# Kernel optimization log

Hardware: AMD Instinct MI355X
Metric: run time of the kernel (lower is better)

## Reference

```python
import jax, jax.numpy as jnp
import numpy as np

N, E, B, D, R, L = 60000, 600000, 512, 128, 30, 3
CUT_LOW, CUT_HIGH = 0.0, 10.0
N_ATOM_TYPES = 100


def _sp(x, beta, threshold):
    # torch.nn.Softplus(beta, threshold): x if beta*x > threshold else log1p(exp(beta*x))/beta
    bx = beta * x
    return jnp.where(bx > threshold, x, jnp.log1p(jnp.exp(jnp.minimum(bx, threshold))) / beta)


def setup_inputs() -> dict:
    key = jax.random.key(0)
    ks = jax.random.split(key, 16)

    def lin(k, fi, fo):
        k1, k2 = jax.random.split(k)
        W = jax.random.normal(k1, (fi, fo), jnp.float32) * (fi ** -0.5)
        b = jax.random.normal(k2, (fo,), jnp.float32) * 0.01
        return W, b

    def lin_stack(k, fi, fo, n):
        Ws, bs = zip(*[lin(kk, fi, fo) for kk in jax.random.split(k, n)])
        return jnp.stack(Ws), jnp.stack(bs)

    inp = {}
    inp['atom_type'] = jax.random.randint(ks[0], (N,), 0, N_ATOM_TYPES)
    inp['src'] = jax.random.randint(ks[1], (E,), 0, N)
    inp['dst'] = jax.random.randint(ks[2], (E,), 0, N)
    inp['graph_ids'] = jnp.sort(jax.random.randint(ks[3], (N,), 0, B))
    inp['dist'] = jax.random.uniform(ks[4], (E,), jnp.float32) * CUT_HIGH
    inp['node_emb'] = jax.random.normal(ks[5], (N_ATOM_TYPES, D), jnp.float32) * 0.1
    inp['W_n1'], inp['b_n1'] = lin_stack(ks[6], D, D, L)
    inp['W_c1'], inp['b_c1'] = lin_stack(ks[7], R, D, L)
    inp['W_c2'], inp['b_c2'] = lin_stack(ks[8], D, D, L)
    inp['W_c3'], inp['b_c3'] = lin_stack(ks[9], D, D, L)
    inp['W_n2'], inp['b_n2'] = lin_stack(ks[10], D, D, L)
    inp['W_n3'], inp['b_n3'] = lin_stack(ks[11], D, D, L)
    inp['W_r1'], inp['b_r1'] = lin(ks[12], D * (L + 1), 64)
    inp['W_r2'], inp['b_r2'] = lin(ks[13], 64, 1)
    return inp


def reference(atom_type, src, dst, graph_ids, dist, node_emb,
              W_n1, b_n1, W_c1, b_c1, W_c2, b_c2, W_c3, b_c3,
              W_n2, b_n2, W_n3, b_n3, W_r1, b_r1, W_r2, b_r2):
    # RBF expansion of edge distances: exp(-(d - mu_k)^2 / gap)  -> [E, R]
    centers = jnp.linspace(CUT_LOW, CUT_HIGH, R).astype(dist.dtype)
    gap = centers[1] - centers[0]
    rbf = jnp.exp(-((dist[:, None] - centers) ** 2) / gap)

    h = node_emb[atom_type]  # node embedding lookup [N, D]
    hs = [h]
    for i in range(L):  # MultiLevelInteraction layers (fixed small count)
        h_new = hs[-1] @ W_n1[i] + b_n1[i]                       # node_layer1 [N, D]
        # VEConv edge MLP on rbf (linear1 -> softplus(0.5,14) -> linear2 -> linear3)
        e = _sp(rbf @ W_c1[i] + b_c1[i], 0.5, 14.0) @ W_c2[i] + b_c2[i]
        e = e @ W_c3[i] + b_c3[i]                                 # [E, D]
        # sum_e(h_new[src]*e) + sum_e(e) fused into one scatter-sum over dst
        msg = (h_new[src] + 1.0) * e                              # [E, D]
        node = jax.ops.segment_sum(msg, dst, num_segments=N)      # [N, D]
        new_node = _sp(node @ W_n2[i] + b_n2[i], 0.5, 14.0) @ W_n3[i] + b_n3[i]
        hs.append(hs[-1] + new_node)                              # residual h_i
    hcat = jnp.concatenate(hs, axis=1)                            # [N, D*(L+1)]
    out = _sp(hcat @ W_r1 + b_r1, 1.0, 20.0) @ W_r2 + b_r2        # [N, 1]
    # dgl.sum_nodes per molecule, then flatten -> [B]
    return jax.ops.segment_sum(out[:, 0], graph_ids, num_segments=B)
```

## Files before the change

kernel.cpp:

```cpp
#include <hip/hip_runtime.h>
#include <math.h>

#define N_NODES 60000
#define N_EDGES 600000
#define B_GRAPHS 512
#define DIM 128
#define RBF_R 30
#define NLAYERS 3
#define NBINS 4096
#define CHUNK 512
#define NCHUNK ((N_NODES + CHUNK - 1) / CHUNK)

typedef __attribute__((ext_vector_type(8))) short bf16x8;
typedef __attribute__((ext_vector_type(4))) float f32x4;

__device__ __forceinline__ float sp05(float x) {
    float bx = 0.5f * x;
    return bx > 14.0f ? x : 2.0f * log1pf(expf(bx));
}
__device__ __forceinline__ float sp1(float x) {
    return x > 20.0f ? x : log1pf(expf(x));
}
__device__ __forceinline__ unsigned short f2bf(float f) {
    unsigned int u = __float_as_uint(f);
    unsigned int r = u + 0x7FFFu + ((u >> 16) & 1u);
    return (unsigned short)(r >> 16);
}
__device__ __forceinline__ float bf2f(unsigned short s) {
    return __uint_as_float(((unsigned int)s) << 16);
}


__global__ void k_convW(const float* __restrict__ Wn1, const float* __restrict__ Wn2,
                        const float* __restrict__ Wn3, unsigned short* __restrict__ WtF) {
    int i = blockIdx.x * 256 + threadIdx.x;
    int mat = i >> 14, r = i & 16383;
    int frag = r >> 9, within = r & 511;
    int ks = frag >> 3, ntile = frag & 7;
    int lane = within >> 3, j = within & 7;
    int q = lane >> 4, l16 = lane & 15;
    int n = ntile * 16 + l16;
    int k = ks * 32 + q * 8 + j;
    const float* src = (mat < 3) ? (Wn1 + (size_t)mat * 16384)
                     : (mat < 6) ? (Wn2 + (size_t)(mat - 3) * 16384)
                                 : (Wn3 + (size_t)(mat - 6) * 16384);
    WtF[i] = f2bf(src[k * 128 + n]);
}

__global__ void k_convR(const float* __restrict__ Wr1, unsigned short* __restrict__ Wr1tF) {
    int i = blockIdx.x * 256 + threadIdx.x;
    int frag = i >> 9, within = i & 511;
    int lvl = frag >> 4, ks = (frag >> 2) & 3, ntile = frag & 3;
    int lane = within >> 3, j = within & 7;
    int q = lane >> 4, l16 = lane & 15;
    int n = ntile * 16 + l16;
    int k = lvl * 128 + ks * 32 + q * 8 + j;
    Wr1tF[i] = f2bf(Wr1[k * 64 + n]);
}

__global__ void k_embed(const int* __restrict__ atom_type,
                        const float* __restrict__ node_emb,
                        float* __restrict__ h0, unsigned short* __restrict__ hb0) {
    int i = blockIdx.x * blockDim.x + threadIdx.x;
    if (i >= N_NODES * DIM) return;
    int n = i >> 7, d = i & 127;
    float v = node_emb[atom_type[n] * DIM + d];
    h0[i] = v;
    hb0[i] = f2bf(v);
}


__global__ void k_hist(const int* __restrict__ dst, int* __restrict__ counts) {
    int e = blockIdx.x * blockDim.x + threadIdx.x;
    if (e >= N_EDGES) return;
    atomicAdd(&counts[dst[e]], 1);
}

__global__ void k_bsum(const int* __restrict__ counts, int* __restrict__ bsums) {
    __shared__ int red[256];
    int c = blockIdx.x, tid = threadIdx.x;
    int base = c * CHUNK;
    int v = 0;
    for (int i = tid; i < CHUNK; i += 256)
        if (base + i < N_NODES) v += counts[base + i];
    red[tid] = v;
    __syncthreads();
    for (int s = 128; s > 0; s >>= 1) {
        if (tid < s) red[tid] += red[tid + s];
        __syncthreads();
    }
    if (tid == 0) bsums[c] = red[0];
}

__global__ void k_scan_b(int* __restrict__ bsums) {
    __shared__ int sb[NCHUNK];
    int tid = threadIdx.x;
    if (tid < NCHUNK) sb[tid] = bsums[tid];
    __syncthreads();
    if (tid == 0) {
        int run = 0;
        for (int i = 0; i < NCHUNK; ++i) { int v = sb[i]; sb[i] = run; run += v; }
    }
    __syncthreads();
    if (tid < NCHUNK) bsums[tid] = sb[tid];
}

__global__ void k_scan_final(const int* __restrict__ counts, const int* __restrict__ bsums,
                             int* __restrict__ offsets) {
    __shared__ int sc[CHUNK];
    int c = blockIdx.x, tid = threadIdx.x;
    int base = c * CHUNK;
    for (int i = tid; i < CHUNK; i += 256)
        sc[i] = (base + i < N_NODES) ? counts[base + i] : 0;
    __syncthreads();
    if (tid == 0) {
        int run = bsums[c];
        for (int i = 0; i < CHUNK; ++i) { int v = sc[i]; sc[i] = run; run += v; }
    }
    __syncthreads();
    for (int i = tid; i < CHUNK; i += 256)
        if (base + i < N_NODES) offsets[base + i] = sc[i];
    if (c == 0 && tid == 0) offsets[N_NODES] = N_EDGES;
}

__global__ void k_fill(const int* __restrict__ src, const int* __restrict__ dst,
                       const float* __restrict__ dist,
                       const int* __restrict__ offsets, int* __restrict__ cnt2,
                       int* __restrict__ srcp, int* __restrict__ binp,
                       float* __restrict__ wp) {
    int e = blockIdx.x * blockDim.x + threadIdx.x;
    if (e >= N_EDGES) return;
    int d = dst[e];
    int pos = offsets[d] + atomicAdd(&cnt2[d], 1);
    srcp[pos] = src[e];
    float x = dist[e];
    float p = x * ((float)NBINS / 10.0f);
    int bin = (int)p;
    if (bin > NBINS - 1) bin = NBINS - 1;
    binp[pos] = bin;
    wp[pos] = p - (float)bin;
}


__global__ void k_table(const float* __restrict__ Wc1, const float* __restrict__ bc1,
                        const float* __restrict__ Wc2, const float* __restrict__ bc2,
                        const float* __restrict__ Wc3, const float* __restrict__ bc3,
                        unsigned short* __restrict__ tableb) {
    __shared__ float t[DIM];
    __shared__ float u[DIM];
    int b = blockIdx.x;
    int d = threadIdx.x;
    float dist = (float)b * (10.0f / (float)NBINS);
    const float gap = 10.0f / 29.0f;
    float acc = bc1[d];
#pragma unroll
    for (int k = 0; k < RBF_R; ++k) {
        float c = (float)k * (10.0f / 29.0f);
        float df = dist - c;
        acc += expf(-df * df / gap) * Wc1[k * DIM + d];
    }
    t[d] = sp05(acc);
    __syncthreads();
    acc = bc2[d];
#pragma unroll 8
    for (int k = 0; k < DIM; ++k) acc += t[k] * Wc2[k * DIM + d];
    u[d] = acc;
    __syncthreads();
    acc = bc3[d];
#pragma unroll 8
    for (int k = 0; k < DIM; ++k) acc += u[k] * Wc3[k * DIM + d];
    tableb[b * DIM + d] = f2bf(acc);
}

__global__ __launch_bounds__(256) void k_gemm_g(const unsigned short* __restrict__ Ab,
                                                const unsigned short* __restrict__ WtF,
                                                const float* __restrict__ bias,
                                                unsigned short* __restrict__ Cb) {
    int tid = threadIdx.x;
    int wave = tid >> 6, lane = tid & 63;
    int q = lane >> 4, l16 = lane & 15;
    int mhalf = wave & 1, nhalf = wave >> 1;
    int rb = blockIdx.x * 64 + mhalf * 32;
    int c0 = nhalf * 64;
    bf16x8 bfrag[4][4];
#pragma unroll
    for (int ks = 0; ks < 4; ++ks)
#pragma unroll
        for (int nt = 0; nt < 4; ++nt)
            bfrag[ks][nt] = *(const bf16x8*)&WtF[(size_t)(ks * 8 + nhalf * 4 + nt) * 512 + lane * 8];
    f32x4 acc[2][4] = {};
#pragma unroll
    for (int ks = 0; ks < 4; ++ks)
#pragma unroll
        for (int mt = 0; mt < 2; ++mt) {
            int m = rb + mt * 16 + l16;
            if (m > N_NODES - 1) m = N_NODES - 1;
            bf16x8 a = *(const bf16x8*)&Ab[(size_t)m * 128 + ks * 32 + q * 8];
#pragma unroll
            for (int nt = 0; nt < 4; ++nt)
                acc[mt][nt] = __builtin_amdgcn_mfma_f32_16x16x32_bf16(a, bfrag[ks][nt], acc[mt][nt], 0, 0, 0);
        }
#pragma unroll
    for (int mt = 0; mt < 2; ++mt)
#pragma unroll
        for (int nt = 0; nt < 4; ++nt) {
            int col = c0 + nt * 16 + l16;
            float b = bias[col] + 1.0f;
#pragma unroll
            for (int r = 0; r < 4; ++r) {
                int row = rb + mt * 16 + q * 4 + r;
                if (row < N_NODES) Cb[(size_t)row * 128 + col] = f2bf(acc[mt][nt][r] + b);
            }
        }
}

__global__ void k_gather(const int* __restrict__ offsets,
                         const int* __restrict__ srcp, const int* __restrict__ binp,
                         const float* __restrict__ wp,
                         const unsigned short* __restrict__ tableb,
                         const unsigned short* __restrict__ gb,
                         unsigned short* __restrict__ nodeb) {
    __shared__ int s_s[128];
    __shared__ int s_bin[128];
    __shared__ float s_w[128];
    int n = blockIdx.x;
    int d = threadIdx.x;
    int beg = offsets[n], end = offsets[n + 1];
    float acc = 0.0f;
    for (int base = beg; base < end; base += 128) {
        int cnt = min(128, end - base);
        if (d < cnt) {
            s_s[d] = srcp[base + d];
            s_bin[d] = binp[base + d];
            s_w[d] = wp[base + d];
        }
        __syncthreads();
        for (int j = 0; j < cnt; ++j) {
            int s = s_s[j];
            int bin = s_bin[j];
            float w = s_w[j];
            float a = bf2f(tableb[(size_t)bin * DIM + d]);
            float b = bf2f(tableb[(size_t)(bin + 1) * DIM + d]);
            float gv = bf2f(gb[(size_t)s * DIM + d]);
            acc += gv * (a + w * (b - a));
        }
        __syncthreads();
    }
    nodeb[(size_t)n * DIM + d] = f2bf(acc);
}

__global__ __launch_bounds__(256) void k_node_update(
    const unsigned short* __restrict__ nodeb,
    const unsigned short* __restrict__ W2tF, const float* __restrict__ b2,
    const unsigned short* __restrict__ W3tF, const float* __restrict__ b3,
    const float* __restrict__ h_in, float* __restrict__ h_out,
    unsigned short* __restrict__ hb_out) {
    __shared__ unsigned short ts[64][136];
    int tid = threadIdx.x;
    int wave = tid >> 6, lane = tid & 63;
    int q = lane >> 4, l16 = lane & 15;
    int mhalf = wave & 1, nhalf = wave >> 1;
    int rb = blockIdx.x * 64 + mhalf * 32;
    int c0 = nhalf * 64;

    bf16x8 bfrag[4][4];
#pragma unroll
    for (int ks = 0; ks < 4; ++ks)
#pragma unroll
        for (int nt = 0; nt < 4; ++nt)
            bfrag[ks][nt] = *(const bf16x8*)&W2tF[(size_t)(ks * 8 + nhalf * 4 + nt) * 512 + lane * 8];
    f32x4 acc[2][4] = {};
#pragma unroll
    for (int ks = 0; ks < 4; ++ks)
#pragma unroll
        for (int mt = 0; mt < 2; ++mt) {
            int m = rb + mt * 16 + l16;
            if (m > N_NODES - 1) m = N_NODES - 1;
            bf16x8 a = *(const bf16x8*)&nodeb[(size_t)m * 128 + ks * 32 + q * 8];
#pragma unroll
            for (int nt = 0; nt < 4; ++nt)
                acc[mt][nt] = __builtin_amdgcn_mfma_f32_16x16x32_bf16(a, bfrag[ks][nt], acc[mt][nt], 0, 0, 0);
        }
#pragma unroll
    for (int mt = 0; mt < 2; ++mt)
#pragma unroll
        for (int nt = 0; nt < 4; ++nt) {
            int col = c0 + nt * 16 + l16;
            float b = b2[col];
#pragma unroll
            for (int r = 0; r < 4; ++r) {
                int lrow = mhalf * 32 + mt * 16 + q * 4 + r;
                ts[lrow][col] = f2bf(sp05(acc[mt][nt][r] + b));
            }
        }
    __syncthreads();
#pragma unroll
    for (int ks = 0; ks < 4; ++ks)
#pragma unroll
        for (int nt = 0; nt < 4; ++nt)
            bfrag[ks][nt] = *(const bf16x8*)&W3tF[(size_t)(ks * 8 + nhalf * 4 + nt) * 512 + lane * 8];
#pragma unroll
    for (int mt = 0; mt < 2; ++mt)
#pragma unroll
        for (int nt = 0; nt < 4; ++nt) acc[mt][nt] = (f32x4){0.f, 0.f, 0.f, 0.f};
#pragma unroll
    for (int ks = 0; ks < 4; ++ks)
#pragma unroll
        for (int mt = 0; mt < 2; ++mt) {
            int lrow = mhalf * 32 + mt * 16 + l16;
            bf16x8 a = *(const bf16x8*)&ts[lrow][ks * 32 + q * 8];
#pragma unroll
            for (int nt = 0; nt < 4; ++nt)
                acc[mt][nt] = __builtin_amdgcn_mfma_f32_16x16x32_bf16(a, bfrag[ks][nt], acc[mt][nt], 0, 0, 0);
        }
#pragma unroll
    for (int mt = 0; mt < 2; ++mt)
#pragma unroll
        for (int nt = 0; nt < 4; ++nt) {
            int col = c0 + nt * 16 + l16;
            float b = b3[col];
#pragma unroll
            for (int r = 0; r < 4; ++r) {
                int row = rb + mt * 16 + q * 4 + r;
                if (row < N_NODES) {
                    size_t idx = (size_t)row * 128 + col;
                    float v = h_in[idx] + acc[mt][nt][r] + b;
                    h_out[idx] = v;
                    hb_out[idx] = f2bf(v);
                }
            }
        }
}

__global__ __launch_bounds__(256) void k_readout(
    const unsigned short* __restrict__ hb0, const unsigned short* __restrict__ hb1,
    const unsigned short* __restrict__ hb2, const unsigned short* __restrict__ hb3,
    const unsigned short* __restrict__ Wr1tF, const float* __restrict__ br1,
    const float* __restrict__ Wr2, const float* __restrict__ br2,
    const int* __restrict__ graph_ids, float* __restrict__ out) {
    int tid = threadIdx.x;
    int wave = tid >> 6, lane = tid & 63;
    int q = lane >> 4, l16 = lane & 15;
    int rb0 = blockIdx.x * 128 + wave * 16;
    const unsigned short* hbs[4] = {hb0, hb1, hb2, hb3};
    f32x4 acc[2][4] = {};
    for (int lvl = 0; lvl < 4; ++lvl) {
        bf16x8 bfrag[4][4];
#pragma unroll
        for (int ks = 0; ks < 4; ++ks)
#pragma unroll
            for (int nt = 0; nt < 4; ++nt)
                bfrag[ks][nt] = *(const bf16x8*)&Wr1tF[(size_t)((lvl * 4 + ks) * 4 + nt) * 512 + lane * 8];
        const unsigned short* Ab = hbs[lvl];
#pragma unroll
        for (int ks = 0; ks < 4; ++ks)
#pragma unroll
            for (int mt = 0; mt < 2; ++mt) {
                int m = rb0 + mt * 64 + l16;
                if (m > N_NODES - 1) m = N_NODES - 1;
                bf16x8 a = *(const bf16x8*)&Ab[(size_t)m * 128 + ks * 32 + q * 8];
#pragma unroll
                for (int nt = 0; nt < 4; ++nt)
                    acc[mt][nt] = __builtin_amdgcn_mfma_f32_16x16x32_bf16(a, bfrag[ks][nt], acc[mt][nt], 0, 0, 0);
            }
    }
    float brr = br2[0];
#pragma unroll
    for (int mt = 0; mt < 2; ++mt) {
        float partial[4] = {0.f, 0.f, 0.f, 0.f};
#pragma unroll
        for (int nt = 0; nt < 4; ++nt) {
            int col = nt * 16 + l16;
            float b = br1[col];
            float w = Wr2[col];
#pragma unroll
            for (int r = 0; r < 4; ++r) partial[r] += sp1(acc[mt][nt][r] + b) * w;
        }
#pragma unroll
        for (int r = 0; r < 4; ++r) {
            float v = partial[r];
            v += __shfl_xor(v, 1); v += __shfl_xor(v, 2);
            v += __shfl_xor(v, 4); v += __shfl_xor(v, 8);
            if (l16 == 0) {
                int row = rb0 + mt * 64 + q * 4 + r;
                if (row < N_NODES) atomicAdd(&out[graph_ids[row]], v + brr);
            }
        }
    }
}

extern "C" void kernel_launch(void* const* d_in, const int* in_sizes, int n_in,
                              void* d_out, int out_size, void* d_ws, size_t ws_size,
                              hipStream_t stream) {
    const int* atom_type   = (const int*)d_in[0];
    const int* src         = (const int*)d_in[1];
    const int* dst         = (const int*)d_in[2];
    const int* graph_ids   = (const int*)d_in[3];
    const float* dist      = (const float*)d_in[4];
    const float* node_emb  = (const float*)d_in[5];
    const float* W_n1 = (const float*)d_in[6];  const float* b_n1 = (const float*)d_in[7];
    const float* W_c1 = (const float*)d_in[8];  const float* b_c1 = (const float*)d_in[9];
    const float* W_c2 = (const float*)d_in[10]; const float* b_c2 = (const float*)d_in[11];
    const float* W_c3 = (const float*)d_in[12]; const float* b_c3 = (const float*)d_in[13];
    const float* W_n2 = (const float*)d_in[14]; const float* b_n2 = (const float*)d_in[15];
    const float* W_n3 = (const float*)d_in[16]; const float* b_n3 = (const float*)d_in[17];
    const float* W_r1 = (const float*)d_in[18]; const float* b_r1 = (const float*)d_in[19];
    const float* W_r2 = (const float*)d_in[20]; const float* b_r2 = (const float*)d_in[21];
    float* out = (float*)d_out;

    size_t ND = (size_t)N_NODES * DIM;
    float* h_even = (float*)d_ws;
    float* h_odd  = h_even + ND;
    float* wp     = h_odd + ND;
    int* offsets  = (int*)(wp + N_EDGES);
    int* srcp     = offsets + 60008;
    int* binp     = srcp + N_EDGES;
    int* counts   = binp + N_EDGES;
    int* cnt2     = counts + N_NODES;
    int* bsums    = cnt2 + N_NODES;
    unsigned short* hb0    = (unsigned short*)(bsums + 128);
    unsigned short* hb1    = hb0 + ND;
    unsigned short* hb2    = hb1 + ND;
    unsigned short* hb3    = hb2 + ND;
    unsigned short* gb     = hb3 + ND;
    unsigned short* nodeb  = gb + ND;
    unsigned short* tableb = nodeb + ND;
    unsigned short* WtF    = tableb + (size_t)(NBINS + 1) * DIM;
    unsigned short* Wr1tF  = WtF + 9 * 16384;

    unsigned short* hbp[4] = {hb0, hb1, hb2, hb3};
    float* hcur = h_even;
    float* hnext = h_odd;

    hipMemsetAsync(out, 0, B_GRAPHS * sizeof(float), stream);
    hipMemsetAsync(counts, 0, (2 * N_NODES + 128) * sizeof(int), stream);

    k_convW<<<(9 * 16384) / 256, 256, 0, stream>>>(W_n1, W_n2, W_n3, WtF);
    k_convR<<<32768 / 256, 256, 0, stream>>>(W_r1, Wr1tF);
    k_embed<<<(N_NODES * DIM) / 256, 256, 0, stream>>>(atom_type, node_emb, h_even, hb0);

    k_hist<<<(N_EDGES + 255) / 256, 256, 0, stream>>>(dst, counts);
    k_bsum<<<NCHUNK, 256, 0, stream>>>(counts, bsums);
    k_scan_b<<<1, 128, 0, stream>>>(bsums);
    k_scan_final<<<NCHUNK, 256, 0, stream>>>(counts, bsums, offsets);
    k_fill<<<(N_EDGES + 255) / 256, 256, 0, stream>>>(src, dst, dist, offsets, cnt2,
                                                      srcp, binp, wp);

    int gblocks = (N_NODES + 63) / 64;
    int rblocks = (N_NODES + 127) / 128;
    for (int i = 0; i < NLAYERS; ++i) {
        k_table<<<NBINS + 1, DIM, 0, stream>>>(
            W_c1 + (size_t)i * RBF_R * DIM, b_c1 + (size_t)i * DIM,
            W_c2 + (size_t)i * DIM * DIM,  b_c2 + (size_t)i * DIM,
            W_c3 + (size_t)i * DIM * DIM,  b_c3 + (size_t)i * DIM, tableb);
        k_gemm_g<<<gblocks, 256, 0, stream>>>(
            hbp[i], WtF + (size_t)i * 16384, b_n1 + (size_t)i * DIM, gb);
        k_gather<<<N_NODES, 128, 0, stream>>>(offsets, srcp, binp, wp, tableb, gb, nodeb);
        k_node_update<<<gblocks, 256, 0, stream>>>(
            nodeb, WtF + (size_t)(3 + i) * 16384, b_n2 + (size_t)i * DIM,
            WtF + (size_t)(6 + i) * 16384, b_n3 + (size_t)i * DIM,
            hcur, hnext, hbp[i + 1]);
        float* tmp = hcur; hcur = hnext; hnext = tmp;
    }
    k_readout<<<rblocks, 256, 0, stream>>>(
        hb0, hb1, hb2, hb3, Wr1tF, b_r1, W_r2, b_r2, graph_ids, out);
}
```

Baseline: 658.1 us.

## Shrink RBF table, pack interpolation pairs, wave-per-node gather, smaller readout tiles

Cuts the precomputed edge-filter table from 4096 to 1024 bins, which shrinks the per-layer table MLP work and keeps the table cache-resident. A new pack kernel stores each bin as a bf16 base value plus a bf16 delta to the next bin, so interpolation needs one 32-bit load. The gather kernel now assigns one wavefront per destination node, with each lane handling two features via 32-bit loads. It is unrolled two edges at a time and no longer uses shared memory or block barriers. Readout blocks now cover 64 rows instead of 128, giving more blocks; the coarser table and bf16 delta lower accuracy.

```diff
diff --git a/kernel.cpp b/kernel.cpp
--- a/kernel.cpp
+++ b/kernel.cpp
@@ -7,7 +7,7 @@
 #define DIM 128
 #define RBF_R 30
 #define NLAYERS 3
-#define NBINS 4096
+#define NBINS 1024
 #define CHUNK 512
 #define NCHUNK ((N_NODES + CHUNK - 1) / CHUNK)
 
@@ -26,8 +26,8 @@
     unsigned int r = u + 0x7FFFu + ((u >> 16) & 1u);
     return (unsigned short)(r >> 16);
 }
-__device__ __forceinline__ float bf2f(unsigned short s) {
-    return __uint_as_float(((unsigned int)s) << 16);
+__device__ __forceinline__ float bf2f(unsigned int s) {
+    return __uint_as_float(s << 16);
 }
 
 
@@ -172,6 +172,14 @@
     tableb[b * DIM + d] = f2bf(acc);
 }
 
+__global__ void k_pack(const unsigned short* __restrict__ tableb,
+                       unsigned int* __restrict__ packed) {
+    int i = blockIdx.x * 256 + threadIdx.x;
+    float a = bf2f(tableb[i]);
+    float b = bf2f(tableb[i + DIM]);
+    packed[i] = (unsigned int)f2bf(a) | ((unsigned int)f2bf(b - a) << 16);
+}
+
 __global__ __launch_bounds__(256) void k_gemm_g(const unsigned short* __restrict__ Ab,
                                                 const unsigned short* __restrict__ WtF,
                                                 const float* __restrict__ bias,
@@ -214,39 +222,41 @@
         }
 }
 
-__global__ void k_gather(const int* __restrict__ offsets,
-                         const int* __restrict__ srcp, const int* __restrict__ binp,
-                         const float* __restrict__ wp,
-                         const unsigned short* __restrict__ tableb,
-                         const unsigned short* __restrict__ gb,
-                         unsigned short* __restrict__ nodeb) {
-    __shared__ int s_s[128];
-    __shared__ int s_bin[128];
-    __shared__ float s_w[128];
-    int n = blockIdx.x;
-    int d = threadIdx.x;
+__global__ __launch_bounds__(256) void k_gather(
+    const int* __restrict__ offsets, const int* __restrict__ srcp,
+    const int* __restrict__ binp, const float* __restrict__ wp,
+    const unsigned int* __restrict__ packed, const unsigned short* __restrict__ gb,
+    unsigned short* __restrict__ nodeb) {
+    int wave = threadIdx.x >> 6, lane = threadIdx.x & 63;
+    int n = blockIdx.x * 4 + wave;
     int beg = offsets[n], end = offsets[n + 1];
-    float acc = 0.0f;
-    for (int base = beg; base < end; base += 128) {
-        int cnt = min(128, end - base);
-        if (d < cnt) {
-            s_s[d] = srcp[base + d];
-            s_bin[d] = binp[base + d];
-            s_w[d] = wp[base + d];
-        }
-        __syncthreads();
-        for (int j = 0; j < cnt; ++j) {
-            int s = s_s[j];
-            int bin = s_bin[j];
-            float w = s_w[j];
-            float a = bf2f(tableb[(size_t)bin * DIM + d]);
-            float b = bf2f(tableb[(size_t)(bin + 1) * DIM + d]);
-            float gv = bf2f(gb[(size_t)s * DIM + d]);
-            acc += gv * (a + w * (b - a));
-        }
-        __syncthreads();
-    }
-    nodeb[(size_t)n * DIM + d] = f2bf(acc);
+    float acc0 = 0.f, acc1 = 0.f, acc2 = 0.f, acc3 = 0.f;
+    int j = beg;
+    for (; j + 2 <= end; j += 2) {
+        int s0 = srcp[j],   s1 = srcp[j + 1];
+        int b0 = binp[j],   b1 = binp[j + 1];
+        float w0 = wp[j],   w1 = wp[j + 1];
+        uint2 p0 = *(const uint2*)&packed[(size_t)b0 * DIM + lane * 2];
+        uint2 p1 = *(const uint2*)&packed[(size_t)b1 * DIM + lane * 2];
+        unsigned int g0 = *(const unsigned int*)&gb[(size_t)s0 * DIM + lane * 2];
+        unsigned int g1 = *(const unsigned int*)&gb[(size_t)s1 * DIM + lane * 2];
+        acc0 += bf2f(g0 & 0xffff) * (bf2f(p0.x & 0xffff) + w0 * bf2f(p0.x >> 16));
+        acc1 += bf2f(g0 >> 16)    * (bf2f(p0.y & 0xffff) + w0 * bf2f(p0.y >> 16));
+        acc2 += bf2f(g1 & 0xffff) * (bf2f(p1.x & 0xffff) + w1 * bf2f(p1.x >> 16));
+        acc3 += bf2f(g1 >> 16)    * (bf2f(p1.y & 0xffff) + w1 * bf2f(p1.y >> 16));
+    }
+    if (j < end) {
+        int s0 = srcp[j];
+        int b0 = binp[j];
+        float w0 = wp[j];
+        uint2 p0 = *(const uint2*)&packed[(size_t)b0 * DIM + lane * 2];
+        unsigned int g0 = *(const unsigned int*)&gb[(size_t)s0 * DIM + lane * 2];
+        acc0 += bf2f(g0 & 0xffff) * (bf2f(p0.x & 0xffff) + w0 * bf2f(p0.x >> 16));
+        acc1 += bf2f(g0 >> 16)    * (bf2f(p0.y & 0xffff) + w0 * bf2f(p0.y >> 16));
+    }
+    acc0 += acc2; acc1 += acc3;
+    unsigned int o = (unsigned int)f2bf(acc0) | ((unsigned int)f2bf(acc1) << 16);
+    *(unsigned int*)&nodeb[(size_t)n * DIM + lane * 2] = o;
 }
 
 __global__ __launch_bounds__(256) void k_node_update(
@@ -341,9 +351,9 @@
     int tid = threadIdx.x;
     int wave = tid >> 6, lane = tid & 63;
     int q = lane >> 4, l16 = lane & 15;
-    int rb0 = blockIdx.x * 128 + wave * 16;
+    int rb = blockIdx.x * 64 + wave * 16;
     const unsigned short* hbs[4] = {hb0, hb1, hb2, hb3};
-    f32x4 acc[2][4] = {};
+    f32x4 acc[4] = {};
     for (int lvl = 0; lvl < 4; ++lvl) {
         bf16x8 bfrag[4][4];
 #pragma unroll
@@ -353,38 +363,33 @@
                 bfrag[ks][nt] = *(const bf16x8*)&Wr1tF[(size_t)((lvl * 4 + ks) * 4 + nt) * 512 + lane * 8];
         const unsigned short* Ab = hbs[lvl];
 #pragma unroll
-        for (int ks = 0; ks < 4; ++ks)
-#pragma unroll
-            for (int mt = 0; mt < 2; ++mt) {
-                int m = rb0 + mt * 64 + l16;
-                if (m > N_NODES - 1) m = N_NODES - 1;
-                bf16x8 a = *(const bf16x8*)&Ab[(size_t)m * 128 + ks * 32 + q * 8];
-#pragma unroll
-                for (int nt = 0; nt < 4; ++nt)
-                    acc[mt][nt] = __builtin_amdgcn_mfma_f32_16x16x32_bf16(a, bfrag[ks][nt], acc[mt][nt], 0, 0, 0);
-            }
+        for (int ks = 0; ks < 4; ++ks) {
+            int m = rb + l16;
+            if (m > N_NODES - 1) m = N_NODES - 1;
+            bf16x8 a = *(const bf16x8*)&Ab[(size_t)m * 128 + ks * 32 + q * 8];
+#pragma unroll
+            for (int nt = 0; nt < 4; ++nt)
+                acc[nt] = __builtin_amdgcn_mfma_f32_16x16x32_bf16(a, bfrag[ks][nt], acc[nt], 0, 0, 0);
+        }
     }
     float brr = br2[0];
-#pragma unroll
-    for (int mt = 0; mt < 2; ++mt) {
-        float partial[4] = {0.f, 0.f, 0.f, 0.f};
-#pragma unroll
-        for (int nt = 0; nt < 4; ++nt) {
-            int col = nt * 16 + l16;
-            float b = br1[col];
-            float w = Wr2[col];
-#pragma unroll
-            for (int r = 0; r < 4; ++r) partial[r] += sp1(acc[mt][nt][r] + b) * w;
-        }
-#pragma unroll
-        for (int r = 0; r < 4; ++r) {
-            float v = partial[r];
-            v += __shfl_xor(v, 1); v += __shfl_xor(v, 2);
-            v += __shfl_xor(v, 4); v += __shfl_xor(v, 8);
-            if (l16 == 0) {
-                int row = rb0 + mt * 64 + q * 4 + r;
-                if (row < N_NODES) atomicAdd(&out[graph_ids[row]], v + brr);
-            }
+    float partial[4] = {0.f, 0.f, 0.f, 0.f};
+#pragma unroll
+    for (int nt = 0; nt < 4; ++nt) {
+        int col = nt * 16 + l16;
+        float b = br1[col];
+        float w = Wr2[col];
+#pragma unroll
+        for (int r = 0; r < 4; ++r) partial[r] += sp1(acc[nt][r] + b) * w;
+    }
+#pragma unroll
+    for (int r = 0; r < 4; ++r) {
+        float v = partial[r];
+        v += __shfl_xor(v, 1); v += __shfl_xor(v, 2);
+        v += __shfl_xor(v, 4); v += __shfl_xor(v, 8);
+        if (l16 == 0) {
+            int row = rb + q * 4 + r;
+            if (row < N_NODES) atomicAdd(&out[graph_ids[row]], v + brr);
         }
     }
 }
@@ -418,7 +423,8 @@
     int* counts   = binp + N_EDGES;
     int* cnt2     = counts + N_NODES;
     int* bsums    = cnt2 + N_NODES;
-    unsigned short* hb0    = (unsigned short*)(bsums + 128);
+    unsigned int* packed = (unsigned int*)(bsums + 128);
+    unsigned short* hb0    = (unsigned short*)(packed + (size_t)NBINS * DIM);
     unsigned short* hb1    = hb0 + ND;
     unsigned short* hb2    = hb1 + ND;
     unsigned short* hb3    = hb2 + ND;
@@ -447,21 +453,21 @@
                                                       srcp, binp, wp);
 
     int gblocks = (N_NODES + 63) / 64;
-    int rblocks = (N_NODES + 127) / 128;
     for (int i = 0; i < NLAYERS; ++i) {
         k_table<<<NBINS + 1, DIM, 0, stream>>>(
             W_c1 + (size_t)i * RBF_R * DIM, b_c1 + (size_t)i * DIM,
             W_c2 + (size_t)i * DIM * DIM,  b_c2 + (size_t)i * DIM,
             W_c3 + (size_t)i * DIM * DIM,  b_c3 + (size_t)i * DIM, tableb);
+        k_pack<<<(NBINS * DIM) / 256, 256, 0, stream>>>(tableb, packed);
         k_gemm_g<<<gblocks, 256, 0, stream>>>(
             hbp[i], WtF + (size_t)i * 16384, b_n1 + (size_t)i * DIM, gb);
-        k_gather<<<N_NODES, 128, 0, stream>>>(offsets, srcp, binp, wp, tableb, gb, nodeb);
+        k_gather<<<N_NODES / 4, 256, 0, stream>>>(offsets, srcp, binp, wp, packed, gb, nodeb);
         k_node_update<<<gblocks, 256, 0, stream>>>(
             nodeb, WtF + (size_t)(3 + i) * 16384, b_n2 + (size_t)i * DIM,
             WtF + (size_t)(6 + i) * 16384, b_n3 + (size_t)i * DIM,
             hcur, hnext, hbp[i + 1]);
         float* tmp = hcur; hcur = hnext; hnext = tmp;
     }
-    k_readout<<<rblocks, 256, 0, stream>>>(
+    k_readout<<<gblocks, 256, 0, stream>>>(
         hb0, hb1, hb2, hb3, Wr1tF, b_r1, W_r2, b_r2, graph_ids, out);
 }
```

Result: no change. 669.8 us (+1.8%).
